# Kernel tuning notes

Hardware: AMD Instinct MI355X
Metric: run time of the kernel (lower is better)

The kernel has to match this reference:

```python
import math
import jax, jax.numpy as jnp
import numpy as np

B, S, H = 8, 1024, 1024
NH = 16
HD = H // NH  # 64


def setup_inputs() -> dict:
    key = jax.random.key(0)
    k1, k2, k3, k4 = jax.random.split(key, 4)
    hidden_states = jax.random.normal(k1, (B, S, H), dtype=jnp.float32)
    attention_mask = jax.random.randint(k2, (B, 1, 1, S), 0, 2, dtype=jnp.int32)
    w_qkv = jax.random.normal(k3, (H, 3 * H), dtype=jnp.float32) * (1.0 / math.sqrt(H))
    b_qkv = jax.random.normal(k4, (3 * H,), dtype=jnp.float32) * 0.02
    return {"hidden_states": hidden_states, "attention_mask": attention_mask,
            "w_qkv": w_qkv, "b_qkv": b_qkv}


def reference(hidden_states, attention_mask, w_qkv, b_qkv):
    b, s, _ = hidden_states.shape
    # fused QKV projection: [b, s, 3H]
    qkv = jnp.einsum('bsh,hk->bsk', hidden_states, w_qkv) + b_qkv
    # view (b, s, nh, 3*hd) -> permute -> chunk last dim (per-head q|k|v layout)
    qkv = qkv.reshape(b, s, NH, 3, HD)
    qkv = jnp.transpose(qkv, (0, 2, 1, 3, 4))      # [b, nh, s, 3, hd]
    q, k, v = qkv[..., 0, :], qkv[..., 1, :], qkv[..., 2, :]
    # raw scores, then FusedScaleMaskSoftmax semantics: scale * scores, mask, fp32 softmax
    scores = jnp.einsum('bhqd,bhkd->bhqk', q, k)
    scale = math.sqrt(HD)  # module passes sqrt(head_dim) as multiplicative scale
    scores = scores.astype(jnp.float32) * scale
    mask = attention_mask != 0                     # nonzero -> masked (padding)
    scores = jnp.where(mask, jnp.float32(-10000.0), scores)
    probs = jax.nn.softmax(scores, axis=-1).astype(hidden_states.dtype)
    # dropout prob = 0 -> identity
    context = jnp.einsum('bhqk,bhkd->bhqd', probs, v)
    context = jnp.transpose(context, (0, 2, 1, 3)).reshape(b, s, NH * HD)
    return context
```

## Files before the change

### kernel.cpp

```cpp
#include <hip/hip_runtime.h>
#include <math.h>

#define Bdim 8
#define Sdim 1024
#define Hdim 1024
#define NHd 16
#define HDd 64
#define N3H 3072

#define Q_OFF   0u
#define K_OFF   16777216u
#define V_OFF   33554432u
#define WH_OFF  41943040u
#define WL_OFF  45088768u
#define AHI_OFF 0u
#define ALO_OFF 8388608u

typedef __bf16 bf16x8 __attribute__((ext_vector_type(8)));
typedef float  f32x4  __attribute__((ext_vector_type(4)));

__device__ __forceinline__ unsigned short f2bf(float x) {
  unsigned b = __builtin_bit_cast(unsigned, x);
  return (unsigned short)((b + 0x7FFFu + ((b >> 16) & 1u)) >> 16);
}
__device__ __forceinline__ float bf2f(unsigned short h) {
  unsigned b = ((unsigned)h) << 16;
  return __builtin_bit_cast(float, b);
}
__device__ __forceinline__ void split_hl(float v, unsigned short& h, unsigned short& l) {
  h = f2bf(v);
  l = f2bf(v - bf2f(h));
}
__device__ __forceinline__ void async16(void* lds, const void* g) {
  __builtin_amdgcn_global_load_lds((const __attribute__((address_space(1))) unsigned int*)g,
                                   (__attribute__((address_space(3))) unsigned int*)lds, 16, 0, 0);
}

__global__ __launch_bounds__(256) void convert_AW(
    const float* __restrict__ A, const float* __restrict__ W,
    unsigned short* __restrict__ aout, unsigned short* __restrict__ ws)
{
  __shared__ float T[64][65];
  const int tid = threadIdx.x;
  int bid = blockIdx.x;
  if (bid < 4096) {
    size_t i = ((size_t)bid * 256 + tid) * 8;
    float4 a0 = *(const float4*)&A[i];
    float4 a1 = *(const float4*)&A[i + 4];
    float av[8] = {a0.x, a0.y, a0.z, a0.w, a1.x, a1.y, a1.z, a1.w};
    unsigned short h[8], l[8];
    #pragma unroll
    for (int j = 0; j < 8; ++j) split_hl(av[j], h[j], l[j]);
    *(uint4*)&aout[AHI_OFF + i] = *(uint4*)h;
    *(uint4*)&aout[ALO_OFF + i] = *(uint4*)l;
    return;
  }
  bid -= 4096;
  const int n0 = (bid % (N3H / 64)) * 64;
  const int k0 = (bid / (N3H / 64)) * 64;
  #pragma unroll
  for (int r = 0; r < 4; ++r) {
    int k = r * 16 + (tid >> 4);
    int n = (tid & 15) * 4;
    float4 v = *(const float4*)&W[(size_t)(k0 + k) * N3H + n0 + n];
    T[k][n + 0] = v.x; T[k][n + 1] = v.y; T[k][n + 2] = v.z; T[k][n + 3] = v.w;
  }
  __syncthreads();
  int n = tid >> 2;
  int kl = (tid & 3) * 16;
  unsigned short h[16], l[16];
  #pragma unroll
  for (int i = 0; i < 16; ++i) split_hl(T[kl + i][n], h[i], l[i]);
  size_t base = (size_t)(n0 + n) * 1024 + k0 + kl;
  *(uint4*)&ws[WH_OFF + base]     = *(uint4*)&h[0];
  *(uint4*)&ws[WH_OFF + base + 8] = *(uint4*)&h[8];
  *(uint4*)&ws[WL_OFF + base]     = *(uint4*)&l[0];
  *(uint4*)&ws[WL_OFF + base + 8] = *(uint4*)&l[8];
}

__global__ __launch_bounds__(256, 2) void qkv_mfma(
    const unsigned short* __restrict__ ao,
    const unsigned short* __restrict__ ws,
    const float* __restrict__ bias,
    unsigned short* __restrict__ wso)
{
  __shared__ unsigned short sA[2][128 * 32];
  __shared__ unsigned short sB[2][128 * 32];

  const int tid  = threadIdx.x;
  const int wave = tid >> 6;
  const int lane = tid & 63;
  const int l16  = lane & 15;
  const int quad = lane >> 4;

  const int n0 = blockIdx.x * 128;
  const int m0 = blockIdx.y * 128;
  const int wm = (wave >> 1) * 64;
  const int wn = (wave & 1) * 64;

  const unsigned short* Ah = ao + AHI_OFF;
  const unsigned short* Al = ao + ALO_OFF;
  const unsigned short* Wh = ws + WH_OFF;
  const unsigned short* Wl = ws + WL_OFF;

  f32x4 acc[4][4];
  #pragma unroll
  for (int i = 0; i < 4; ++i)
    #pragma unroll
    for (int j = 0; j < 4; ++j) acc[i][j] = (f32x4){0.f, 0.f, 0.f, 0.f};

  for (int kt = 0; kt < 1024; kt += 32) {
    __syncthreads();
    #pragma unroll
    for (int r = 0; r < 2; ++r) {
      int chunk = r * 256 + tid;
      int row = chunk >> 2;
      int c8  = (chunk & 3) << 3;
      int ldsoff = (r * 256 + wave * 64) * 8;
      async16(&sA[0][ldsoff], &Ah[(size_t)(m0 + row) * 1024 + kt + c8]);
      async16(&sA[1][ldsoff], &Al[(size_t)(m0 + row) * 1024 + kt + c8]);
      async16(&sB[0][ldsoff], &Wh[(size_t)(n0 + row) * 1024 + kt + c8]);
      async16(&sB[1][ldsoff], &Wl[(size_t)(n0 + row) * 1024 + kt + c8]);
    }
    __syncthreads();

    bf16x8 af[4][2], bf[4][2];
    #pragma unroll
    for (int i = 0; i < 4; ++i) {
      int row = wm + i * 16 + l16;
      af[i][0] = *(const bf16x8*)&sA[0][row * 32 + quad * 8];
      af[i][1] = *(const bf16x8*)&sA[1][row * 32 + quad * 8];
    }
    #pragma unroll
    for (int j = 0; j < 4; ++j) {
      int row = wn + j * 16 + l16;
      bf[j][0] = *(const bf16x8*)&sB[0][row * 32 + quad * 8];
      bf[j][1] = *(const bf16x8*)&sB[1][row * 32 + quad * 8];
    }
    #pragma unroll
    for (int i = 0; i < 4; ++i)
      #pragma unroll
      for (int j = 0; j < 4; ++j) {
        acc[i][j] = __builtin_amdgcn_mfma_f32_16x16x32_bf16(af[i][0], bf[j][0], acc[i][j], 0, 0, 0);
        acc[i][j] = __builtin_amdgcn_mfma_f32_16x16x32_bf16(af[i][1], bf[j][0], acc[i][j], 0, 0, 0);
        acc[i][j] = __builtin_amdgcn_mfma_f32_16x16x32_bf16(af[i][0], bf[j][1], acc[i][j], 0, 0, 0);
      }
  }

  const int ncol0 = n0 + wn;
  const int which = (ncol0 >> 6) % 3;
  const int head  = ncol0 / 192;
  const int mrow0 = m0 + wm;
  const int bb = mrow0 >> 10;
  const int sb = mrow0 & 1023;
  const int bh = bb * NHd + head;

  float bs[4];
  #pragma unroll
  for (int j = 0; j < 4; ++j) bs[j] = bias[ncol0 + j * 16 + l16];

  if (which == 0) {
    unsigned short* dst = wso + Q_OFF + ((size_t)bh * Sdim + sb) * 128;
    #pragma unroll
    for (int i = 0; i < 4; ++i)
      #pragma unroll
      for (int j = 0; j < 4; ++j) {
        int d = j * 16 + l16;
        #pragma unroll
        for (int r = 0; r < 4; ++r) {
          int s = i * 16 + quad * 4 + r;
          unsigned short h, l;
          split_hl(acc[i][j][r] + bs[j], h, l);
          dst[(size_t)s * 128 + d]      = h;
          dst[(size_t)s * 128 + 64 + d] = l;
        }
      }
  } else if (which == 1) {
    unsigned short* dst = wso + K_OFF + (size_t)bh * 131072 + (size_t)(sb >> 6) * 8192;
    #pragma unroll
    for (int i = 0; i < 4; ++i)
      #pragma unroll
      for (int j = 0; j < 4; ++j) {
        int c = j * 16 + l16;
        #pragma unroll
        for (int r = 0; r < 4; ++r) {
          int sp = i * 16 + quad * 4 + r;
          int idx = ((((sp >> 4) * 4 + (c >> 5)) * 64 + ((c >> 3) & 3) * 16 + (sp & 15)) << 3) + (c & 7);
          unsigned short h, l;
          split_hl(acc[i][j][r] + bs[j], h, l);
          dst[idx]        = h;
          dst[idx + 1024] = l;
        }
      }
  } else {
    unsigned short* dst = wso + V_OFF + (size_t)bh * 65536 + (size_t)(sb >> 6) * 4096;
    #pragma unroll
    for (int i = 0; i < 4; ++i)
      #pragma unroll
      for (int j = 0; j < 4; ++j) {
        int dr = j * 16 + l16;
        int ky = i * 16 + quad * 4;
        int idx = ((((dr >> 4) * 2 + (ky >> 5)) * 64 + ((ky >> 3) & 3) * 16 + (dr & 15)) << 3) + (ky & 7);
        unsigned short p[4];
        #pragma unroll
        for (int r = 0; r < 4; ++r) p[r] = f2bf(acc[i][j][r] + bs[j]);
        *(uint2*)&dst[idx] = *(uint2*)p;
      }
  }
}

__global__ __launch_bounds__(256, 2) void attn_mfma(
    const unsigned short* __restrict__ qhl,
    const unsigned short* __restrict__ khl,
    const unsigned short* __restrict__ vt,
    const int* __restrict__ mask,
    float* __restrict__ out)
{
  __shared__ unsigned short Ks[2][8192];
  __shared__ unsigned short Vs[2][4096];
  __shared__ unsigned short Pw[4][1024];
  __shared__ float msks[1024];

  const int tid  = threadIdx.x;
  const int wave = tid >> 6;
  const int lane = tid & 63;
  const int l16  = lane & 15;
  const int quad = lane >> 4;

  const int qt = blockIdx.x & 15;
  const int bh = blockIdx.x >> 4;
  const int bb = bh >> 4;
  const int q0 = qt * 64;

  const unsigned short* kplane = khl + (size_t)bh * 131072;
  const unsigned short* vplane = vt  + (size_t)bh * 65536;

  #pragma unroll
  for (int r = 0; r < 4; ++r)
    async16(&Ks[0][(r * 256 + tid) * 8], &kplane[(size_t)(r * 256 + tid) * 8]);
  #pragma unroll
  for (int r = 0; r < 2; ++r)
    async16(&Vs[0][(r * 256 + tid) * 8], &vplane[(size_t)(r * 256 + tid) * 8]);

  {
    int4 mv = *(const int4*)&mask[bb * Sdim + tid * 4];
    msks[tid * 4 + 0] = mv.x ? 1.f : 0.f;
    msks[tid * 4 + 1] = mv.y ? 1.f : 0.f;
    msks[tid * 4 + 2] = mv.z ? 1.f : 0.f;
    msks[tid * 4 + 3] = mv.w ? 1.f : 0.f;
  }

  bf16x8 qf[4];
  {
    int row = q0 + wave * 16 + l16;
    const unsigned short* src = qhl + ((size_t)bh * Sdim + row) * 128;
    #pragma unroll
    for (int kk = 0; kk < 4; ++kk)
      qf[kk] = *(const bf16x8*)&src[kk * 32 + quad * 8];
  }

  f32x4 O[4] = {{0.f,0.f,0.f,0.f},{0.f,0.f,0.f,0.f},{0.f,0.f,0.f,0.f},{0.f,0.f,0.f,0.f}};
  float mrow[4] = {-INFINITY, -INFINITY, -INFINITY, -INFINITY};
  float lrow[4] = {0.f, 0.f, 0.f, 0.f};

  __syncthreads();

  #pragma unroll 1
  for (int kt = 0; kt < 16; ++kt) {
    const int cur = kt & 1;
    if (kt < 15) {
      const unsigned short* ksrc = kplane + (size_t)(kt + 1) * 8192;
      const unsigned short* vsrc = vplane + (size_t)(kt + 1) * 4096;
      #pragma unroll
      for (int r = 0; r < 4; ++r)
        async16(&Ks[cur ^ 1][(r * 256 + tid) * 8], &ksrc[(size_t)(r * 256 + tid) * 8]);
      #pragma unroll
      for (int r = 0; r < 2; ++r)
        async16(&Vs[cur ^ 1][(r * 256 + tid) * 8], &vsrc[(size_t)(r * 256 + tid) * 8]);
    }

    f32x4 sc[4];
    #pragma unroll
    for (int ns = 0; ns < 4; ++ns) {
      f32x4 c = {0.f, 0.f, 0.f, 0.f};
      bf16x8 kf0 = *(const bf16x8*)&Ks[cur][((ns * 4 + 0) * 64 + lane) * 8];
      bf16x8 kf1 = *(const bf16x8*)&Ks[cur][((ns * 4 + 1) * 64 + lane) * 8];
      bf16x8 kf2 = *(const bf16x8*)&Ks[cur][((ns * 4 + 2) * 64 + lane) * 8];
      bf16x8 kf3 = *(const bf16x8*)&Ks[cur][((ns * 4 + 3) * 64 + lane) * 8];
      c = __builtin_amdgcn_mfma_f32_16x16x32_bf16(qf[0], kf0, c, 0, 0, 0);
      c = __builtin_amdgcn_mfma_f32_16x16x32_bf16(qf[1], kf1, c, 0, 0, 0);
      c = __builtin_amdgcn_mfma_f32_16x16x32_bf16(qf[2], kf0, c, 0, 0, 0);
      c = __builtin_amdgcn_mfma_f32_16x16x32_bf16(qf[3], kf1, c, 0, 0, 0);
      c = __builtin_amdgcn_mfma_f32_16x16x32_bf16(qf[0], kf2, c, 0, 0, 0);
      c = __builtin_amdgcn_mfma_f32_16x16x32_bf16(qf[1], kf3, c, 0, 0, 0);
      sc[ns] = c;
    }

    float rmax[4] = {-INFINITY, -INFINITY, -INFINITY, -INFINITY};
    #pragma unroll
    for (int ns = 0; ns < 4; ++ns) {
      float mk = msks[kt * 64 + ns * 16 + l16];
      #pragma unroll
      for (int r = 0; r < 4; ++r) {
        float s = (mk != 0.f) ? -10000.f : sc[ns][r] * 8.f;
        sc[ns][r] = s;
        rmax[r] = fmaxf(rmax[r], s);
      }
    }
    #pragma unroll
    for (int r = 0; r < 4; ++r) {
      float v = rmax[r];
      v = fmaxf(v, __shfl_xor(v, 1, 16));
      v = fmaxf(v, __shfl_xor(v, 2, 16));
      v = fmaxf(v, __shfl_xor(v, 4, 16));
      v = fmaxf(v, __shfl_xor(v, 8, 16));
      rmax[r] = v;
    }

    float alpha[4];
    #pragma unroll
    for (int r = 0; r < 4; ++r) {
      float mn = fmaxf(mrow[r], rmax[r]);
      alpha[r] = __expf(mrow[r] - mn);
      mrow[r] = mn;
      lrow[r] *= alpha[r];
    }
    #pragma unroll
    for (int d = 0; d < 4; ++d)
      #pragma unroll
      for (int r = 0; r < 4; ++r) O[d][r] *= alpha[r];

    float rsum[4] = {0.f, 0.f, 0.f, 0.f};
    #pragma unroll
    for (int ns = 0; ns < 4; ++ns) {
      int key = ns * 16 + l16;
      int cbase = (((key >> 5) * 4 + ((key >> 3) & 3)) * 16 + quad * 4) * 8 + (key & 7);
      #pragma unroll
      for (int r = 0; r < 4; ++r) {
        float p = __expf(sc[ns][r] - mrow[r]);
        rsum[r] += p;
        Pw[wave][cbase + r * 8] = f2bf(p);
      }
    }
    #pragma unroll
    for (int r = 0; r < 4; ++r) {
      float v = rsum[r];
      v += __shfl_xor(v, 1, 16);
      v += __shfl_xor(v, 2, 16);
      v += __shfl_xor(v, 4, 16);
      v += __shfl_xor(v, 8, 16);
      lrow[r] += v;
    }

    bf16x8 pf[2];
    #pragma unroll
    for (int kk = 0; kk < 2; ++kk)
      pf[kk] = *(const bf16x8*)&Pw[wave][((kk * 4 + quad) * 16 + l16) * 8];
    #pragma unroll
    for (int d = 0; d < 4; ++d)
      #pragma unroll
      for (int kk = 0; kk < 2; ++kk) {
        bf16x8 vf = *(const bf16x8*)&Vs[cur][((d * 2 + kk) * 64 + lane) * 8];
        O[d] = __builtin_amdgcn_mfma_f32_16x16x32_bf16(pf[kk], vf, O[d], 0, 0, 0);
      }

    __syncthreads();
  }

  const int h = bh & 15;
  #pragma unroll
  for (int r = 0; r < 4; ++r) {
    float inv = 1.f / lrow[r];
    int q = q0 + wave * 16 + quad * 4 + r;
    float* dst = out + ((size_t)bb * Sdim + q) * Hdim + h * HDd;
    #pragma unroll
    for (int d = 0; d < 4; ++d)
      dst[d * 16 + l16] = O[d][r] * inv;
  }
}

extern "C" void kernel_launch(void* const* d_in, const int* in_sizes, int n_in,
                              void* d_out, int out_size, void* d_ws, size_t ws_size,
                              hipStream_t stream) {
  const float* hs   = (const float*)d_in[0];
  const int*   mask = (const int*)d_in[1];
  const float* w    = (const float*)d_in[2];
  const float* bias = (const float*)d_in[3];
  float* out = (float*)d_out;
  unsigned short* ws = (unsigned short*)d_ws;
  unsigned short* ao = (unsigned short*)d_out;

  convert_AW<<<4096 + (N3H / 64) * (1024 / 64), 256, 0, stream>>>(hs, w, ao, ws);

  qkv_mfma<<<dim3(N3H / 128, 8192 / 128), 256, 0, stream>>>(ao, ws, bias, ws);

  attn_mfma<<<Bdim * NHd * (Sdim / 64), 256, 0, stream>>>(
      ws + Q_OFF, ws + K_OFF, ws + V_OFF, mask, out);
}
```

Measured before the change: 395.5 us.

## Single-buffer K/V tiles, raise occupancy, and swap block index ordering

Drops the K/V double buffer in shared memory and raises the launch-bounds occupancy target from 2 to 4 blocks per CU. Loads now happen synchronously at the top of each iteration between two barriers. The blockIdx decomposition is also swapped so consecutive blocks cover different batch-heads at the same query tile. The aim is to hide latency through more resident waves instead of software prefetch, at the cost of losing load/compute overlap within a block, adding barriers, and possibly hurting K/V cache locality.

```diff
diff --git a/kernel.cpp b/kernel.cpp
--- a/kernel.cpp
+++ b/kernel.cpp
@@ -209,15 +209,15 @@
   }
 }
 
-__global__ __launch_bounds__(256, 2) void attn_mfma(
+__global__ __launch_bounds__(256, 4) void attn_mfma(
     const unsigned short* __restrict__ qhl,
     const unsigned short* __restrict__ khl,
     const unsigned short* __restrict__ vt,
     const int* __restrict__ mask,
     float* __restrict__ out)
 {
-  __shared__ unsigned short Ks[2][8192];
-  __shared__ unsigned short Vs[2][4096];
+  __shared__ unsigned short Ks[8192];
+  __shared__ unsigned short Vs[4096];
   __shared__ unsigned short Pw[4][1024];
   __shared__ float msks[1024];
 
@@ -227,20 +227,13 @@
   const int l16  = lane & 15;
   const int quad = lane >> 4;
 
-  const int qt = blockIdx.x & 15;
-  const int bh = blockIdx.x >> 4;
+  const int bh = blockIdx.x & 127;
+  const int qt = blockIdx.x >> 7;
   const int bb = bh >> 4;
   const int q0 = qt * 64;
 
   const unsigned short* kplane = khl + (size_t)bh * 131072;
   const unsigned short* vplane = vt  + (size_t)bh * 65536;
-
-  #pragma unroll
-  for (int r = 0; r < 4; ++r)
-    async16(&Ks[0][(r * 256 + tid) * 8], &kplane[(size_t)(r * 256 + tid) * 8]);
-  #pragma unroll
-  for (int r = 0; r < 2; ++r)
-    async16(&Vs[0][(r * 256 + tid) * 8], &vplane[(size_t)(r * 256 + tid) * 8]);
 
   {
     int4 mv = *(const int4*)&mask[bb * Sdim + tid * 4];
@@ -263,30 +256,29 @@
   float mrow[4] = {-INFINITY, -INFINITY, -INFINITY, -INFINITY};
   float lrow[4] = {0.f, 0.f, 0.f, 0.f};
 
-  __syncthreads();
-
   #pragma unroll 1
   for (int kt = 0; kt < 16; ++kt) {
-    const int cur = kt & 1;
-    if (kt < 15) {
-      const unsigned short* ksrc = kplane + (size_t)(kt + 1) * 8192;
-      const unsigned short* vsrc = vplane + (size_t)(kt + 1) * 4096;
+    __syncthreads();
+    {
+      const unsigned short* ksrc = kplane + (size_t)kt * 8192;
+      const unsigned short* vsrc = vplane + (size_t)kt * 4096;
       #pragma unroll
       for (int r = 0; r < 4; ++r)
-        async16(&Ks[cur ^ 1][(r * 256 + tid) * 8], &ksrc[(size_t)(r * 256 + tid) * 8]);
+        async16(&Ks[(r * 256 + tid) * 8], &ksrc[(size_t)(r * 256 + tid) * 8]);
       #pragma unroll
       for (int r = 0; r < 2; ++r)
-        async16(&Vs[cur ^ 1][(r * 256 + tid) * 8], &vsrc[(size_t)(r * 256 + tid) * 8]);
-    }
+        async16(&Vs[(r * 256 + tid) * 8], &vsrc[(size_t)(r * 256 + tid) * 8]);
+    }
+    __syncthreads();
 
     f32x4 sc[4];
     #pragma unroll
     for (int ns = 0; ns < 4; ++ns) {
       f32x4 c = {0.f, 0.f, 0.f, 0.f};
-      bf16x8 kf0 = *(const bf16x8*)&Ks[cur][((ns * 4 + 0) * 64 + lane) * 8];
-      bf16x8 kf1 = *(const bf16x8*)&Ks[cur][((ns * 4 + 1) * 64 + lane) * 8];
-      bf16x8 kf2 = *(const bf16x8*)&Ks[cur][((ns * 4 + 2) * 64 + lane) * 8];
-      bf16x8 kf3 = *(const bf16x8*)&Ks[cur][((ns * 4 + 3) * 64 + lane) * 8];
+      bf16x8 kf0 = *(const bf16x8*)&Ks[((ns * 4 + 0) * 64 + lane) * 8];
+      bf16x8 kf1 = *(const bf16x8*)&Ks[((ns * 4 + 1) * 64 + lane) * 8];
+      bf16x8 kf2 = *(const bf16x8*)&Ks[((ns * 4 + 2) * 64 + lane) * 8];
+      bf16x8 kf3 = *(const bf16x8*)&Ks[((ns * 4 + 3) * 64 + lane) * 8];
       c = __builtin_amdgcn_mfma_f32_16x16x32_bf16(qf[0], kf0, c, 0, 0, 0);
       c = __builtin_amdgcn_mfma_f32_16x16x32_bf16(qf[1], kf1, c, 0, 0, 0);
       c = __builtin_amdgcn_mfma_f32_16x16x32_bf16(qf[2], kf0, c, 0, 0, 0);
@@ -360,11 +352,9 @@
     for (int d = 0; d < 4; ++d)
       #pragma unroll
       for (int kk = 0; kk < 2; ++kk) {
-        bf16x8 vf = *(const bf16x8*)&Vs[cur][((d * 2 + kk) * 64 + lane) * 8];
+        bf16x8 vf = *(const bf16x8*)&Vs[((d * 2 + kk) * 64 + lane) * 8];
         O[d] = __builtin_amdgcn_mfma_f32_16x16x32_bf16(pf[kk], vf, O[d], 0, 0, 0);
       }
-
-    __syncthreads();
   }
 
   const int h = bh & 15;
```

Measured after the change: 361.5 us. -8.6%, faster.
